# Kernel optimization log

Measured on AMD Instinct MI355X. Metric: run time of the kernel, lower is better.

## Reference

```python
import jax, jax.numpy as jnp
import numpy as np

B, CIN, COUT, L, K, HEADS, GROUPS, EPS = 16, 256, 512, 1024, 3, 8, 32, 1e-5


def group_norm(x, w, b, groups, eps=EPS):
    Bx, C, Lx = x.shape
    g = x.reshape(Bx, groups, C // groups, Lx)
    mu = g.mean(axis=(2, 3), keepdims=True)
    var = g.var(axis=(2, 3), keepdims=True)
    g = (g - mu) * jax.lax.rsqrt(var + eps)
    return g.reshape(Bx, C, Lx) * w[None, :, None] + b[None, :, None]


def conv1d(x, w, b, pad):
    y = jax.lax.conv_general_dilated(x, w, window_strides=(1,), padding=[(pad, pad)],
                                     dimension_numbers=('NCH', 'OIH', 'NCH'))
    return y + b[None, :, None]


def setup_inputs() -> dict:
    key = jax.random.key(0)
    ks = jax.random.split(key, 12)
    def kn(k, shape, fan_in, scale=1.0):
        return (np.sqrt(1.0 / fan_in) * jax.random.normal(k, shape, dtype=jnp.float32)) * scale
    return {
        'x': jax.random.normal(ks[0], (B, CIN, L), dtype=jnp.float32),
        'norm0_w': jnp.ones((CIN,), jnp.float32), 'norm0_b': jnp.zeros((CIN,), jnp.float32),
        'conv0_w': kn(ks[1], (COUT, CIN, K), CIN * K), 'conv0_b': jnp.zeros((COUT,), jnp.float32),
        'norm1_w': jnp.ones((COUT,), jnp.float32), 'norm1_b': jnp.zeros((COUT,), jnp.float32),
        'conv1_w': kn(ks[2], (COUT, COUT, K), COUT * K, 1e-5), 'conv1_b': jnp.zeros((COUT,), jnp.float32),
        'skip_w': kn(ks[3], (COUT, CIN, 1), CIN), 'skip_b': jnp.zeros((COUT,), jnp.float32),
        'norm2_w': jnp.ones((COUT,), jnp.float32), 'norm2_b': jnp.zeros((COUT,), jnp.float32),
        'qkv_w': kn(ks[4], (COUT * 3, COUT, 1), COUT), 'qkv_b': jnp.zeros((COUT * 3,), jnp.float32),
        'proj_w': kn(ks[5], (COUT, COUT, 1), COUT, 1e-5), 'proj_b': jnp.zeros((COUT,), jnp.float32),
    }


def reference(x, norm0_w, norm0_b, conv0_w, conv0_b, norm1_w, norm1_b, conv1_w, conv1_b,
              skip_w, skip_b, norm2_w, norm2_b, qkv_w, qkv_b, proj_w, proj_b):
    orig = x
    h = conv1d(jax.nn.silu(group_norm(x, norm0_w, norm0_b, min(GROUPS, CIN))), conv0_w, conv0_b, (K - 1) // 2)
    h = jax.nn.silu(group_norm(h, norm1_w, norm1_b, min(GROUPS, COUT)))
    h = conv1d(h, conv1_w, conv1_b, (K - 1) // 2)
    h = h + conv1d(orig, skip_w, skip_b, 0)  # skip (in != out), dropout p=0
    # skip_scale = 1
    # attention: qkv [B, 3C, L] -> [B*H, C/H, 3, L] (channel axis splits as H, C/H, 3)
    qkv = conv1d(group_norm(h, norm2_w, norm2_b, min(GROUPS, COUT)), qkv_w, qkv_b, 0)
    ch = COUT // HEADS
    qkv = qkv.reshape(B * HEADS, ch, 3, L)
    q, k, v = qkv[:, :, 0], qkv[:, :, 1], qkv[:, :, 2]  # each [BH, ch, L]
    scores = jnp.einsum('nci,ncj->nij', q, k) / np.sqrt(ch).astype(np.float32)
    attn = jax.nn.softmax(scores, axis=-1)
    a = jnp.einsum('nij,ncj->nci', attn, v).reshape(B, COUT, L)
    return h + conv1d(a, proj_w, proj_b, 0)
```

## Files before the change

kernel.cpp:

```cpp
#include <hip/hip_runtime.h>


typedef float f32x4 __attribute__((ext_vector_type(4)));
typedef float f32x16 __attribute__((ext_vector_type(16)));
typedef short short8 __attribute__((ext_vector_type(8)));

__device__ __forceinline__ unsigned short f2bf(float f) {
  union { float f; unsigned u; } v; v.f = f;
  return (unsigned short)((v.u + 0x7FFFu + ((v.u >> 16) & 1u)) >> 16);
}
__device__ __forceinline__ float bf2f(unsigned short h) {
  union { unsigned u; float f; } v; v.u = ((unsigned)h) << 16;
  return v.f;
}

__device__ __forceinline__ float fexp2(float x) {
  float r;
  asm("v_exp_f32 %0, %1" : "=v"(r) : "v"(x));
  return r;
}

__device__ __forceinline__ void gload_lds16(const void* g, void* l) {
  __builtin_amdgcn_global_load_lds(
      (const __attribute__((address_space(1))) unsigned int*)g,
      (__attribute__((address_space(3))) unsigned int*)l, 16, 0, 0);
}

__device__ __forceinline__ float swap_add(float x) {
  float a = x, b = x;
  asm("v_permlane32_swap_b32 %0, %1" : "+v"(a), "+v"(b));
  return a + b;
}

__device__ __forceinline__ short8 pack8(float a0, float a1, float a2, float a3,
                                        float a4, float a5, float a6, float a7) {
  unsigned x0, x1, x2, x3;
  asm("v_cvt_pk_bf16_f32 %0, %1, %2" : "=v"(x0) : "v"(a0), "v"(a1));
  asm("v_cvt_pk_bf16_f32 %0, %1, %2" : "=v"(x1) : "v"(a2), "v"(a3));
  asm("v_cvt_pk_bf16_f32 %0, %1, %2" : "=v"(x2) : "v"(a4), "v"(a5));
  asm("v_cvt_pk_bf16_f32 %0, %1, %2" : "=v"(x3) : "v"(a6), "v"(a7));
  asm("v_permlane32_swap_b32 %0, %1" : "+v"(x0), "+v"(x2));
  asm("v_permlane32_swap_b32 %0, %1" : "+v"(x1), "+v"(x3));
  union { unsigned u[4]; short8 s; } r;
  r.u[0] = x0; r.u[1] = x1; r.u[2] = x2; r.u[3] = x3;
  return r.s;
}
#define PACK8(V, B) pack8(V[B+0], V[B+1], V[B+2], V[B+3], V[B+4], V[B+5], V[B+6], V[B+7])

__global__ __launch_bounds__(256) void prep_stats(
    const float* __restrict__ c0w, const float* __restrict__ c1w,
    const float* __restrict__ skw, const float* __restrict__ qw,
    const float* __restrict__ pw,
    unsigned short* __restrict__ WT0, unsigned short* __restrict__ WT1,
    unsigned short* __restrict__ WSK, unsigned short* __restrict__ WQ,
    unsigned short* __restrict__ WP,
    const float* __restrict__ x, float2* __restrict__ mr,
    unsigned short* __restrict__ outT) {
  __shared__ float2 red[4];
  const int t = threadIdx.x;
  if (blockIdx.x >= 9216) {
    const int blk = blockIdx.x - 9216;
    const int g = blk & 31;
    const int bb = blk >> 5;
    const size_t base = ((size_t)bb * 256 + g * 8) * 1024;
    float s = 0.f, ss = 0.f;
#pragma unroll
    for (int i = t * 4; i < 8192; i += 1024) {
      const float4 v = *(const float4*)(x + base + i);
      s += (v.x + v.y) + (v.z + v.w);
      ss += (v.x * v.x + v.y * v.y) + (v.z * v.z + v.w * v.w);
    }
#pragma unroll
    for (int off = 32; off; off >>= 1) {
      s += __shfl_down(s, off);
      ss += __shfl_down(ss, off);
    }
    if ((t & 63) == 0) red[t >> 6] = make_float2(s, ss);
    __syncthreads();
    const float2 r0 = red[0], r1 = red[1], r2 = red[2], r3 = red[3];
    const float tots = (r0.x + r1.x) + (r2.x + r3.x);
    const float totss = (r0.y + r1.y) + (r2.y + r3.y);
    const float mean = tots * (1.f / 8192.f);
    const float var = totss * (1.f / 8192.f) - mean * mean;
    if (t == 0) mr[bb * 32 + g] = make_float2(mean, rsqrtf(var + 1e-5f));
    unsigned short* ob = outT + (size_t)bb * 1026 * 256 + g * 8;
    if (t < 8) {
      ob[t] = 0;
      ob[(size_t)1025 * 256 + t] = 0;
    }
    return;
  }
  int idx = blockIdx.x * 256 + t;
  if (idx < 393216) {
    const int ci = idx & 255; const int rem = idx >> 8;
    const int co = rem & 511; const int kk = rem >> 9;
    WT0[idx] = f2bf(c0w[((size_t)co * 256 + ci) * 3 + kk]); return;
  }
  idx -= 393216;
  if (idx < 786432) {
    const int ci = idx & 511; const int rem = idx >> 9;
    const int co = rem & 511; const int kk = rem >> 9;
    WT1[idx] = f2bf(c1w[((size_t)co * 512 + ci) * 3 + kk]); return;
  }
  idx -= 786432;
  if (idx < 131072) { WSK[idx] = f2bf(skw[idx]); return; }
  idx -= 131072;
  if (idx < 786432) {
    const int ci = idx & 511; const int m = idx >> 9;
    const int s = m >> 9, rem = m & 511, h = rem >> 6, c = rem & 63;
    WQ[idx] = f2bf(qw[((size_t)(h * 192 + c * 3 + s) * 512) + ci]); return;
  }
  idx -= 786432;
  WP[idx] = f2bf(pw[idx]);
}

template<int MODE, bool SILU, int C, bool PADZ, bool RAW, bool IN16>
__global__ __launch_bounds__(256) void nt_kernel(
    const float* __restrict__ in, const float2* __restrict__ st,
    const float* __restrict__ gw, const float* __restrict__ gb,
    unsigned short* __restrict__ outT, unsigned short* __restrict__ rawT) {
  constexpr int CPG = C / 32;
  __shared__ float ls[64][65];
  __shared__ unsigned short lsr[RAW ? 64 : 1][72];
  __shared__ float2 gstat[4];
  const int b = blockIdx.z, c0 = blockIdx.y * 64, l0 = blockIdx.x * 64;
  const int t = threadIdx.x;
  if (MODE == 2) {
    if (t < 4) {
      const int g = (c0 >> 4) + t;
      const float2* p = st + (((size_t)b * 4 + (g >> 3)) * 8 + (g & 7)) * 8;
      float s = 0.f, ss = 0.f;
#pragma unroll
      for (int i = 0; i < 8; ++i) { s += p[i].x; ss += p[i].y; }
      const float mean = s * (1.f / 16384.f);
      const float var = ss * (1.f / 16384.f) - mean * mean;
      gstat[t] = make_float2(mean, rsqrtf(var + 1e-5f));
    }
    __syncthreads();
  }
  const int lw = (t & 15) * 4;
  const int cr = t >> 4;
#pragma unroll
  for (int p = 0; p < 4; ++p) {
    const int c = p * 16 + cr;
    const int cc = c0 + c;
    float sc = 1.f, bi = 0.f;
    if (MODE == 1) {
      const float2 ms = st[b * 32 + cc / CPG];
      sc = gw[cc] * ms.y;
      bi = gb[cc] - ms.x * sc;
    } else if (MODE == 2) {
      const float2 ms = gstat[c >> 4];
      sc = gw[cc] * ms.y;
      bi = gb[cc] - ms.x * sc;
    }
    float4 v;
    if (IN16) {
      const ushort4 u4 = *(const ushort4*)((const unsigned short*)in +
                                           ((size_t)b * C + cc) * 1024 + l0 + lw);
      v = make_float4(bf2f(u4.x), bf2f(u4.y), bf2f(u4.z), bf2f(u4.w));
    } else {
      v = *(const float4*)(in + ((size_t)b * C + cc) * 1024 + l0 + lw);
    }
    if (RAW) {
      lsr[c][lw + 0] = f2bf(v.x);
      lsr[c][lw + 1] = f2bf(v.y);
      lsr[c][lw + 2] = f2bf(v.z);
      lsr[c][lw + 3] = f2bf(v.w);
    }
    float o[4] = {v.x * sc + bi, v.y * sc + bi, v.z * sc + bi, v.w * sc + bi};
    if (SILU) {
#pragma unroll
      for (int d = 0; d < 4; ++d) o[d] = o[d] / (1.f + __expf(-o[d]));
    }
#pragma unroll
    for (int d = 0; d < 4; ++d) ls[c][lw + d] = o[d];
  }
  __syncthreads();
  const int l = t >> 2, c16 = (t & 3) * 16;
  short8 v0, v1;
#pragma unroll
  for (int j = 0; j < 8; ++j) v0[j] = (short)f2bf(ls[c16 + j][l]);
#pragma unroll
  for (int j = 0; j < 8; ++j) v1[j] = (short)f2bf(ls[c16 + 8 + j][l]);
  unsigned short* ob = outT + ((size_t)b * 1026 + l0 + l + 1) * C + c0 + c16;
  *(short8*)ob = v0;
  *(short8*)(ob + 8) = v1;
  if (RAW) {
    short8 w0, w1;
#pragma unroll
    for (int j = 0; j < 8; ++j) w0[j] = (short)lsr[c16 + j][l];
#pragma unroll
    for (int j = 0; j < 8; ++j) w1[j] = (short)lsr[c16 + 8 + j][l];
    unsigned short* rb = rawT + ((size_t)b * 1026 + l0 + l + 1) * C + c0 + c16;
    *(short8*)rb = w0;
    *(short8*)(rb + 8) = w1;
  }
  if (PADZ) {
    const short8 z = {};
    if (blockIdx.x == 0 && t < 8)
      *(short8*)(outT + (size_t)b * 1026 * C + c0 + t * 8) = z;
    if (blockIdx.x == 15 && t < 8)
      *(short8*)(outT + ((size_t)b * 1026 + 1025) * C + c0 + t * 8) = z;
  }
}

__global__ __launch_bounds__(256) void ntE_kernel(
    const unsigned short* __restrict__ Ht, const float2* __restrict__ part,
    const float* __restrict__ gw, const float* __restrict__ gb,
    unsigned short* __restrict__ outT) {
  __shared__ float2 gstat[32];
  const int b = blockIdx.y;
  const int t = threadIdx.x;
  if (t < 32) {
    const float2* p = part + (((size_t)b * 4 + (t >> 3)) * 8 + (t & 7)) * 8;
    float s = 0.f, ss = 0.f;
#pragma unroll
    for (int i = 0; i < 8; ++i) { s += p[i].x; ss += p[i].y; }
    const float mean = s * (1.f / 16384.f);
    const float var = ss * (1.f / 16384.f) - mean * mean;
    gstat[t] = make_float2(mean, rsqrtf(var + 1e-5f));
  }
  __syncthreads();
  const int c8 = t & 63;
  const float2 ms = gstat[c8 >> 1];
  const int cbase = c8 * 8;
  const float4 g0 = *(const float4*)(gw + cbase);
  const float4 g1 = *(const float4*)(gw + cbase + 4);
  const float4 b0 = *(const float4*)(gb + cbase);
  const float4 b1 = *(const float4*)(gb + cbase + 4);
  float sc[8], bi[8];
  sc[0] = g0.x * ms.y; sc[1] = g0.y * ms.y; sc[2] = g0.z * ms.y; sc[3] = g0.w * ms.y;
  sc[4] = g1.x * ms.y; sc[5] = g1.y * ms.y; sc[6] = g1.z * ms.y; sc[7] = g1.w * ms.y;
  bi[0] = b0.x - ms.x * sc[0]; bi[1] = b0.y - ms.x * sc[1];
  bi[2] = b0.z - ms.x * sc[2]; bi[3] = b0.w - ms.x * sc[3];
  bi[4] = b1.x - ms.x * sc[4]; bi[5] = b1.y - ms.x * sc[5];
  bi[6] = b1.z - ms.x * sc[6]; bi[7] = b1.w - ms.x * sc[7];
#pragma unroll
  for (int pass = 0; pass < 4; ++pass) {
    const int lp = blockIdx.x * 16 + pass * 4 + (t >> 6) + 1;
    const size_t o = ((size_t)b * 1026 + lp) * 512 + cbase;
    const short8 v = *(const short8*)(Ht + o);
    short8 r;
#pragma unroll
    for (int e = 0; e < 8; ++e) {
      const float y = bf2f((unsigned short)v[e]) * sc[e] + bi[e];
      r[e] = (short)f2bf(y / (1.f + __expf(-y)));
    }
    *(short8*)(outT + o) = r;
  }
  const short8 z = {};
  if (blockIdx.x == 0 && t < 64)
    *(short8*)(outT + (size_t)b * 1026 * 512 + t * 8) = z;
  if (blockIdx.x == 63 && t < 64)
    *(short8*)(outT + ((size_t)b * 1026 + 1025) * 512 + t * 8) = z;
}

template<int K, bool ADD, bool SCATTER, bool FUSE, bool STATS, bool TROUT,
         bool OUT16, bool ADD16>
__global__ __launch_bounds__(256, 2) void convmm_kernel(
    const unsigned short* __restrict__ Xt, const unsigned short* __restrict__ Wt,
    const float* __restrict__ bias, const float* __restrict__ addsrc,
    float* __restrict__ outp,
    unsigned short* __restrict__ qd, unsigned short* __restrict__ kd,
    unsigned short* __restrict__ vd, int Cin, int Cout,
    const unsigned short* __restrict__ X2, const unsigned short* __restrict__ W2,
    const float* __restrict__ bias2, int Cin2, float2* __restrict__ part) {
  constexpr int XR = (K == 3) ? 160 : 128;
  __shared__ __align__(16) unsigned short smem[K * 128 * 64 + XR * 64];
  unsigned short* wT = smem;
  unsigned short* xT = smem + K * 128 * 64;
  const int t = threadIdx.x, lane = t & 63, w = t >> 6;
  const int b = blockIdx.z, co0 = blockIdx.y * 128, l0 = blockIdx.x * 128;
  const int m0 = (w >> 1) * 64, n0 = (w & 1) * 64;
  const int START = (K == 3) ? l0 : (l0 + 1);
  f32x4 acc[4][4] = {};
  for (int ci0 = 0; ci0 < Cin; ci0 += 64) {
    __syncthreads();
    for (int rr = 0; rr < K * 4; ++rr) {
      const int row = rr * 32 + (t >> 3);
      const int co = row & 127;
      const int c16 = (t & 7) ^ (co & 7);
      gload_lds16(Wt + ((size_t)(row >> 7) * Cout + co0 + co) * Cin + ci0 + c16 * 8,
                  (char*)wT + (rr * 256 + t) * 16);
    }
    for (int rr = 0; rr < XR / 32; ++rr) {
      const int r = rr * 32 + (t >> 3);
      int lp = START + r;
      if (lp > 1025) lp = 1025;
      const int c16 = (t & 7) ^ (r & 7);
      gload_lds16(Xt + ((size_t)b * 1026 + lp) * Cin + ci0 + c16 * 8,
                  (char*)xT + (rr * 256 + t) * 16);
    }
    __syncthreads();
#pragma unroll
    for (int kk = 0; kk < K; ++kk) {
#pragma unroll
      for (int ks = 0; ks < 2; ++ks) {
        short8 af[4], bfr[4];
#pragma unroll
        for (int mf = 0; mf < 4; ++mf) {
          const int row = m0 + mf * 16 + (lane & 15);
          const int u = (kk * 128 + row) * 8 + ((ks * 4 + (lane >> 4)) ^ (row & 7));
          af[mf] = *(const short8*)(wT + u * 8);
        }
#pragma unroll
        for (int nf = 0; nf < 4; ++nf) {
          const int r = n0 + nf * 16 + (lane & 15) + kk;
          const int u = r * 8 + ((ks * 4 + (lane >> 4)) ^ (r & 7));
          bfr[nf] = *(const short8*)(xT + u * 8);
        }
#pragma unroll
        for (int mf = 0; mf < 4; ++mf)
#pragma unroll
          for (int nf = 0; nf < 4; ++nf)
            acc[mf][nf] = __builtin_amdgcn_mfma_f32_16x16x32_bf16(
                af[mf], bfr[nf], acc[mf][nf], 0, 0, 0);
      }
    }
  }
  if (FUSE) {
    for (int ci0 = 0; ci0 < Cin2; ci0 += 64) {
      __syncthreads();
      for (int rr = 0; rr < 4; ++rr) {
        const int co = rr * 32 + (t >> 3);
        const int c16 = (t & 7) ^ (co & 7);
        gload_lds16(W2 + (size_t)(co0 + co) * Cin2 + ci0 + c16 * 8,
                    (char*)wT + (rr * 256 + t) * 16);
      }
      for (int rr = 0; rr < 4; ++rr) {
        const int r = rr * 32 + (t >> 3);
        const int lp = l0 + 1 + r;
        const int c16 = (t & 7) ^ (r & 7);
        gload_lds16(X2 + ((size_t)b * 1026 + lp) * Cin2 + ci0 + c16 * 8,
                    (char*)xT + (rr * 256 + t) * 16);
      }
      __syncthreads();
#pragma unroll
      for (int ks = 0; ks < 2; ++ks) {
        short8 af[4], bfr[4];
#pragma unroll
        for (int mf = 0; mf < 4; ++mf) {
          const int row = m0 + mf * 16 + (lane & 15);
          const int u = row * 8 + ((ks * 4 + (lane >> 4)) ^ (row & 7));
          af[mf] = *(const short8*)(wT + u * 8);
        }
#pragma unroll
        for (int nf = 0; nf < 4; ++nf) {
          const int r = n0 + nf * 16 + (lane & 15);
          const int u = r * 8 + ((ks * 4 + (lane >> 4)) ^ (r & 7));
          bfr[nf] = *(const short8*)(xT + u * 8);
        }
#pragma unroll
        for (int mf = 0; mf < 4; ++mf)
#pragma unroll
          for (int nf = 0; nf < 4; ++nf)
            acc[mf][nf] = __builtin_amdgcn_mfma_f32_16x16x32_bf16(
                af[mf], bfr[nf], acc[mf][nf], 0, 0, 0);
      }
    }
  }
  if (TROUT) {
    __syncthreads();
    unsigned short* TP = smem;
    float2* sr = (float2*)(TP + 128 * 128);
    float sg[4] = {}, ssg[4] = {};
#pragma unroll
    for (int mf = 0; mf < 4; ++mf)
#pragma unroll
      for (int r = 0; r < 4; ++r) {
        const int mloc = m0 + mf * 16 + (lane >> 4) * 4 + r;
        const float bv = bias[co0 + mloc];
#pragma unroll
        for (int nf = 0; nf < 4; ++nf) {
          const int l = n0 + nf * 16 + (lane & 15);
          const float v = acc[mf][nf][r] + bv;
          sg[mf] += v; ssg[mf] += v * v;
          const int u = l * 16 + ((mloc >> 3) ^ (l & 7));
          TP[u * 8 + (mloc & 7)] = f2bf(v);
        }
      }
#pragma unroll
    for (int mf = 0; mf < 4; ++mf) {
      float s = sg[mf], ss = ssg[mf];
#pragma unroll
      for (int off = 32; off; off >>= 1) {
        s += __shfl_down(s, off);
        ss += __shfl_down(ss, off);
      }
      if (lane == 0)
        sr[(((w >> 1) * 4 + mf) << 1) | (w & 1)] = make_float2(s, ss);
    }
    __syncthreads();
    for (int it = 0; it < 8; ++it) {
      const int idx = it * 256 + t;
      const int l = idx >> 4, mu = idx & 15;
      const short8 v = *(const short8*)(TP + (l * 16 + (mu ^ (l & 7))) * 8);
      *(short8*)(qd + ((size_t)b * 1026 + l0 + l + 1) * 512 + co0 + mu * 8) = v;
    }
    if (t < 8) {
      const float2 a = sr[t * 2], c = sr[t * 2 + 1];
      part[(((size_t)b * 4 + blockIdx.y) * 8 + t) * 8 + blockIdx.x] =
          make_float2(a.x + c.x, a.y + c.y);
    }
  } else if (!SCATTER) {
    float sg[4] = {}, ssg[4] = {};
#pragma unroll
    for (int mf = 0; mf < 4; ++mf) {
#pragma unroll
      for (int r = 0; r < 4; ++r) {
        const int co = co0 + m0 + mf * 16 + (lane >> 4) * 4 + r;
        float bv = bias[co];
        if (FUSE) bv += bias2[co];
#pragma unroll
        for (int nf = 0; nf < 4; ++nf) {
          const int l = l0 + n0 + nf * 16 + (lane & 15);
          const size_t o = ((size_t)b * Cout + co) * 1024 + l;
          float v = acc[mf][nf][r] + bv;
          if (ADD) {
            if (ADD16) v += bf2f(((const unsigned short*)addsrc)[o]);
            else       v += addsrc[o];
          }
          if (OUT16) ((unsigned short*)outp)[o] = f2bf(v);
          else       outp[o] = v;
          if (STATS) { sg[mf] += v; ssg[mf] += v * v; }
        }
      }
    }
    if (STATS) {
      __syncthreads();
      float2* sr = (float2*)smem;
#pragma unroll
      for (int mf = 0; mf < 4; ++mf) {
        float s = sg[mf], ss = ssg[mf];
#pragma unroll
        for (int off = 32; off; off >>= 1) {
          s += __shfl_down(s, off);
          ss += __shfl_down(ss, off);
        }
        if (lane == 0)
          sr[(((w >> 1) * 4 + mf) << 1) | (w & 1)] = make_float2(s, ss);
      }
      __syncthreads();
      if (t < 8) {
        const float2 a = sr[t * 2], c = sr[t * 2 + 1];
        part[(((size_t)b * 4 + blockIdx.y) * 8 + t) * 8 + blockIdx.x] =
            make_float2(a.x + c.x, a.y + c.y);
      }
    }
  } else {
    __syncthreads();
    unsigned short* TP = smem;
    const int sidx = co0 >> 9;
    const int mbase = co0 & 511;
    const float qscale = (sidx == 0) ? 0.18033688f : 1.0f;
    if (sidx < 2) {
#pragma unroll
      for (int mf = 0; mf < 4; ++mf)
#pragma unroll
        for (int r = 0; r < 4; ++r) {
          const int mloc = m0 + mf * 16 + (lane >> 4) * 4 + r;
          const int mg = mbase + mloc;
          const float bv = bias[(mg >> 6) * 192 + (mg & 63) * 3 + sidx];
#pragma unroll
          for (int nf = 0; nf < 4; ++nf) {
            const int l = n0 + nf * 16 + (lane & 15);
            const int u = l * 16 + ((mloc >> 3) ^ (l & 7));
            TP[u * 8 + (mloc & 7)] = f2bf((acc[mf][nf][r] + bv) * qscale);
          }
        }
      __syncthreads();
      unsigned short* dst = (sidx == 0) ? qd : kd;
      for (int it = 0; it < 8; ++it) {
        const int idx = it * 256 + t;
        const int l = idx >> 4, mu = idx & 15;
        const int mg = mbase + mu * 8;
        const int bh = b * 8 + (mg >> 6);
        const short8 v = *(const short8*)(TP + (l * 16 + (mu ^ (l & 7))) * 8);
        *(short8*)(dst + ((size_t)bh * 1024 + l0 + l) * 64 + (mg & 63)) = v;
      }
    } else {
#pragma unroll
      for (int mf = 0; mf < 4; ++mf)
#pragma unroll
        for (int r = 0; r < 4; ++r) {
          const int mloc = m0 + mf * 16 + (lane >> 4) * 4 + r;
          const int mg = mbase + mloc;
          const float bv = bias[(mg >> 6) * 192 + (mg & 63) * 3 + 2];
#pragma unroll
          for (int nf = 0; nf < 4; ++nf) {
            const int l = n0 + nf * 16 + (lane & 15);
            const int u = mloc * 16 + ((l >> 3) ^ ((mloc & 7) << 1));
            TP[u * 8 + (l & 7)] = f2bf(acc[mf][nf][r] + bv);
          }
        }
      __syncthreads();
      for (int it = 0; it < 8; ++it) {
        const int idx = it * 256 + t;
        const int mloc = idx >> 4, lu = idx & 15;
        const int mg = mbase + mloc;
        const int bh = b * 8 + (mg >> 6);
        const short8 v =
            *(const short8*)(TP + (mloc * 16 + (lu ^ ((mloc & 7) << 1))) * 8);
        *(short8*)(vd + ((size_t)bh * 64 + (mg & 63)) * 1024 + l0 + lu * 8) = v;
      }
    }
  }
}

__global__ __launch_bounds__(256, 2) void attn_mfma(
    const unsigned short* __restrict__ Qb, const unsigned short* __restrict__ Kb,
    const unsigned short* __restrict__ Vb, unsigned short* __restrict__ Ab) {
  __shared__ __align__(16) unsigned short Ks[2][64 * 64];
  __shared__ __align__(16) unsigned short Vs[2][64 * 64];
  unsigned short* QP = &Ks[0][0];
  const int t = threadIdx.x, lane = t & 63, w = t >> 6;
  const int hi = lane >> 5, l31 = lane & 31;
  const int id = blockIdx.x;
  const int xcd = id & 7, local = id >> 3;
  const int bh = (xcd << 4) | (local >> 2);
  const int b = bh >> 3, h = bh & 7;
  const int iq0 = (local & 3) * 256;
  const unsigned short* Qg = Qb + ((size_t)bh * 1024 + iq0) * 64;
  const unsigned short* Kg = Kb + (size_t)bh * 1024 * 64;
  const unsigned short* Vg = Vb + (size_t)bh * 64 * 1024;
  for (int rr = 0; rr < 8; ++rr) {
    const int r = rr * 32 + (t >> 3), c16 = (t & 7) ^ (r & 7);
    gload_lds16(Qg + (size_t)r * 64 + c16 * 8, (char*)QP + (rr * 256 + t) * 16);
  }
  __syncthreads();
  const int irow0 = w * 64 + l31;
  const int irow1 = w * 64 + 32 + l31;
  short8 qf[2][4];
#pragma unroll
  for (int kc = 0; kc < 4; ++kc) {
    const int u0 = irow0 * 8 + ((kc * 2 + hi) ^ (irow0 & 7));
    const int u1 = irow1 * 8 + ((kc * 2 + hi) ^ (irow1 & 7));
    qf[0][kc] = *(const short8*)(QP + u0 * 8);
    qf[1][kc] = *(const short8*)(QP + u1 * 8);
  }
  __syncthreads();
  for (int rr = 0; rr < 2; ++rr) {
    const int r = rr * 32 + (t >> 3), c16 = (t & 7) ^ (r & 7);
    gload_lds16(Kg + (size_t)r * 64 + c16 * 8, (char*)Ks[0] + (rr * 256 + t) * 16);
    gload_lds16(Vg + (size_t)r * 1024 + c16 * 8, (char*)Vs[0] + (rr * 256 + t) * 16);
  }
  __syncthreads();
  float ls0 = 0.f, ls1 = 0.f;
  f32x16 oA[2][2] = {};
  auto kv_iter = [&](const int ti, const int cur) {
    if (ti < 15) {
      const int j1 = (ti + 1) * 64;
      for (int rr = 0; rr < 2; ++rr) {
        const int r = rr * 32 + (t >> 3), c16 = (t & 7) ^ (r & 7);
        gload_lds16(Kg + (size_t)(j1 + r) * 64 + c16 * 8,
                    (char*)Ks[cur ^ 1] + (rr * 256 + t) * 16);
        gload_lds16(Vg + (size_t)r * 1024 + j1 + c16 * 8,
                    (char*)Vs[cur ^ 1] + (rr * 256 + t) * 16);
      }
    }
    f32x16 s00 = {}, s01 = {}, s10 = {}, s11 = {};
    __builtin_amdgcn_s_setprio(1);
#pragma unroll
    for (int kc = 0; kc < 4; ++kc) {
      const int r0 = l31, r1 = 32 + l31;
      const short8 k0 = *(const short8*)(Ks[cur] + (r0 * 8 + ((kc * 2 + hi) ^ (r0 & 7))) * 8);
      const short8 k1 = *(const short8*)(Ks[cur] + (r1 * 8 + ((kc * 2 + hi) ^ (r1 & 7))) * 8);
      s00 = __builtin_amdgcn_mfma_f32_32x32x16_bf16(k0, qf[0][kc], s00, 0, 0, 0);
      s01 = __builtin_amdgcn_mfma_f32_32x32x16_bf16(k1, qf[0][kc], s01, 0, 0, 0);
      s10 = __builtin_amdgcn_mfma_f32_32x32x16_bf16(k0, qf[1][kc], s10, 0, 0, 0);
      s11 = __builtin_amdgcn_mfma_f32_32x32x16_bf16(k1, qf[1][kc], s11, 0, 0, 0);
    }
    __builtin_amdgcn_s_setprio(0);
    short8 pb0[4], pb1[4];
    {
      float p0 = 0.f, p1 = 0.f, p2 = 0.f, p3 = 0.f;
#pragma unroll
      for (int r = 0; r < 16; ++r) { s00[r] = fexp2(s00[r]); }
#pragma unroll
      for (int r = 0; r < 16; r += 4) {
        p0 += s00[r + 0]; p1 += s00[r + 1]; p2 += s00[r + 2]; p3 += s00[r + 3];
      }
#pragma unroll
      for (int r = 0; r < 16; ++r) { s01[r] = fexp2(s01[r]); }
#pragma unroll
      for (int r = 0; r < 16; r += 4) {
        p0 += s01[r + 0]; p1 += s01[r + 1]; p2 += s01[r + 2]; p3 += s01[r + 3];
      }
      ls0 += (p0 + p1) + (p2 + p3);
      pb0[0] = PACK8(s00, 0); pb0[1] = PACK8(s00, 8);
      pb0[2] = PACK8(s01, 0); pb0[3] = PACK8(s01, 8);
    }
    {
      float p0 = 0.f, p1 = 0.f, p2 = 0.f, p3 = 0.f;
#pragma unroll
      for (int r = 0; r < 16; ++r) { s10[r] = fexp2(s10[r]); }
#pragma unroll
      for (int r = 0; r < 16; r += 4) {
        p0 += s10[r + 0]; p1 += s10[r + 1]; p2 += s10[r + 2]; p3 += s10[r + 3];
      }
#pragma unroll
      for (int r = 0; r < 16; ++r) { s11[r] = fexp2(s11[r]); }
#pragma unroll
      for (int r = 0; r < 16; r += 4) {
        p0 += s11[r + 0]; p1 += s11[r + 1]; p2 += s11[r + 2]; p3 += s11[r + 3];
      }
      ls1 += (p0 + p1) + (p2 + p3);
      pb1[0] = PACK8(s10, 0); pb1[1] = PACK8(s10, 8);
      pb1[2] = PACK8(s11, 0); pb1[3] = PACK8(s11, 8);
    }
    __builtin_amdgcn_s_setprio(1);
#pragma unroll
    for (int cf = 0; cf < 2; ++cf) {
      const int row = cf * 32 + l31;
#pragma unroll
      for (int s = 0; s < 4; ++s) {
        const int u = row * 8 + ((s * 2 + hi) ^ (row & 7));
        const short8 va = *(const short8*)(Vs[cur] + u * 8);
        oA[0][cf] = __builtin_amdgcn_mfma_f32_32x32x16_bf16(va, pb0[s], oA[0][cf], 0, 0, 0);
        oA[1][cf] = __builtin_amdgcn_mfma_f32_32x32x16_bf16(va, pb1[s], oA[1][cf], 0, 0, 0);
      }
    }
    __builtin_amdgcn_s_setprio(0);
    __syncthreads();
  };
  for (int ti = 0; ti < 16; ti += 2) {
    kv_iter(ti, 0);
    kv_iter(ti + 1, 1);
  }
  const float inv0 = 1.f / swap_add(ls0);
  const float inv1 = 1.f / swap_add(ls1);
#pragma unroll
  for (int f = 0; f < 2; ++f) {
    const int irow = f ? irow1 : irow0;
    const float inv = f ? inv1 : inv0;
#pragma unroll
    for (int cf = 0; cf < 2; ++cf)
#pragma unroll
      for (int r = 0; r < 16; ++r) {
        const int c = cf * 32 + (r & 3) + 8 * (r >> 2) + 4 * hi;
        const int u = irow * 8 + ((c >> 3) ^ (irow & 7));
        QP[u * 8 + (c & 7)] = f2bf(oA[f][cf][r] * inv);
      }
  }
  for (int rr = 0; rr < 8; ++rr) {
    const int row = w * 64 + rr * 8 + (lane >> 3);
    const int c16 = lane & 7;
    const int u = row * 8 + (c16 ^ (row & 7));
    const short8 vv = *(const short8*)(QP + u * 8);
    *(short8*)(Ab + ((size_t)b * 1026 + iq0 + row + 1) * 512 + h * 64 + c16 * 8) = vv;
  }
}

#define MB(x) ((size_t)(x) << 20)

extern "C" void kernel_launch(void* const* d_in, const int* in_sizes, int n_in,
                              void* d_out, int out_size, void* d_ws,
                              size_t ws_size, hipStream_t stream) {
  const float* x   = (const float*)d_in[0];
  const float* n0w = (const float*)d_in[1];
  const float* n0b = (const float*)d_in[2];
  const float* c0w = (const float*)d_in[3];
  const float* c0b = (const float*)d_in[4];
  const float* n1w = (const float*)d_in[5];
  const float* n1b = (const float*)d_in[6];
  const float* c1w = (const float*)d_in[7];
  const float* c1b = (const float*)d_in[8];
  const float* skw = (const float*)d_in[9];
  const float* skb = (const float*)d_in[10];
  const float* n2w = (const float*)d_in[11];
  const float* n2b = (const float*)d_in[12];
  const float* qw  = (const float*)d_in[13];
  const float* qb  = (const float*)d_in[14];
  const float* pw  = (const float*)d_in[15];
  const float* pb  = (const float*)d_in[16];
  char* wsb = (char*)d_ws;
  unsigned short* WT0 = (unsigned short*)(wsb);
  unsigned short* WT1 = (unsigned short*)(wsb + MB(1));
  unsigned short* WSK = (unsigned short*)(wsb + MB(3));
  unsigned short* WQ  = (unsigned short*)(wsb + MB(4));
  unsigned short* WP  = (unsigned short*)(wsb + MB(6));
  unsigned short* H2b = (unsigned short*)(wsb + MB(7));
  unsigned short* Qb2 = (unsigned short*)(wsb + MB(41));
  unsigned short* Kb2 = (unsigned short*)(wsb + MB(58));
  unsigned short* H0t = (unsigned short*)(wsb + MB(75));
  unsigned short* Vb2 = (unsigned short*)(wsb + MB(75));
  unsigned short* Xt2 = (unsigned short*)(wsb + MB(92));
  unsigned short* Xt0 = (unsigned short*)(wsb + MB(109));
  unsigned short* Xt1 = (unsigned short*)(wsb + MB(109));
  unsigned short* Ab  = (unsigned short*)(wsb + MB(109));
  unsigned short* Xbf = (unsigned short*)(wsb + MB(126));
  float2* MR0   = (float2*)(wsb + MB(135));
  float2* PART1 = (float2*)(wsb + MB(135) + 8192);
  float2* PART2 = (float2*)(wsb + MB(135) + 32768);
  float* outp = (float*)d_out;

  prep_stats<<<9728, 256, 0, stream>>>(c0w, c1w, skw, qw, pw,
                                       WT0, WT1, WSK, WQ, WP, x, MR0, Xt0);
  nt_kernel<1, true, 256, false, true, false><<<dim3(16, 4, 16), 256, 0, stream>>>(
      x, MR0, n0w, n0b, Xt0, Xbf);
  convmm_kernel<3, false, false, false, true, true, false, false>
      <<<dim3(8, 4, 16), 256, 0, stream>>>(
      Xt0, WT0, c0b, nullptr, nullptr, H0t, nullptr, nullptr, 256, 512,
      nullptr, nullptr, nullptr, 0, PART1);
  ntE_kernel<<<dim3(64, 16), 256, 0, stream>>>(H0t, PART1, n1w, n1b, Xt1);
  convmm_kernel<3, false, false, true, true, false, true, false>
      <<<dim3(8, 4, 16), 256, 0, stream>>>(
      Xt1, WT1, c1b, nullptr, (float*)H2b, nullptr, nullptr, nullptr, 512, 512,
      Xbf, WSK, skb, 256, PART2);
  nt_kernel<2, false, 512, false, false, true><<<dim3(16, 8, 16), 256, 0, stream>>>(
      (const float*)H2b, PART2, n2w, n2b, Xt2, nullptr);
  convmm_kernel<1, false, true, false, false, false, false, false>
      <<<dim3(8, 12, 16), 256, 0, stream>>>(
      Xt2, WQ, qb, nullptr, nullptr, Qb2, Kb2, Vb2, 512, 1536,
      nullptr, nullptr, nullptr, 0, nullptr);
  attn_mfma<<<dim3(512), 256, 0, stream>>>(Qb2, Kb2, Vb2, Ab);
  convmm_kernel<1, true, false, false, false, false, false, true>
      <<<dim3(8, 4, 16), 256, 0, stream>>>(
      Ab, WP, pb, (const float*)H2b, outp, nullptr, nullptr, nullptr, 512, 512,
      nullptr, nullptr, nullptr, 0, nullptr);
}
```

Before: 176.3 us.

## Double-buffer K=1 conv GEMM loads and interleave softmax with PV MFMAs

For the K=1 (pointwise) conv GEMM path, shared-memory staging becomes double-buffered. The next 64-channel slice is prefetched while MFMAs run on the current one, and one barrier per step replaces the two used before. In the attention inner loop, V fragments are loaded once up front and the first PV MFMA batch is issued before the second softmax exp block, so exp work can overlap matrix ops. The setprio hints around PV are dropped. The costs are more LDS per block (which may limit occupancy) and higher register pressure from holding all V fragments.

Result: slower. 184.7 us (+4.8%).

```diff
diff --git a/kernel.cpp b/kernel.cpp
--- a/kernel.cpp
+++ b/kernel.cpp
@@ -266,76 +266,40 @@
     unsigned short* __restrict__ vd, int Cin, int Cout,
     const unsigned short* __restrict__ X2, const unsigned short* __restrict__ W2,
     const float* __restrict__ bias2, int Cin2, float2* __restrict__ part) {
-  constexpr int XR = (K == 3) ? 160 : 128;
-  __shared__ __align__(16) unsigned short smem[K * 128 * 64 + XR * 64];
-  unsigned short* wT = smem;
-  unsigned short* xT = smem + K * 128 * 64;
+  constexpr int XR = 160;
+  constexpr int SMEM_SHORTS = (K == 3) ? (3 * 128 * 64 + XR * 64)
+                                       : (2 * (128 * 64 + 128 * 64));
+  __shared__ __align__(16) unsigned short smem[SMEM_SHORTS];
   const int t = threadIdx.x, lane = t & 63, w = t >> 6;
   const int b = blockIdx.z, co0 = blockIdx.y * 128, l0 = blockIdx.x * 128;
   const int m0 = (w >> 1) * 64, n0 = (w & 1) * 64;
-  const int START = (K == 3) ? l0 : (l0 + 1);
   f32x4 acc[4][4] = {};
-  for (int ci0 = 0; ci0 < Cin; ci0 += 64) {
-    __syncthreads();
-    for (int rr = 0; rr < K * 4; ++rr) {
-      const int row = rr * 32 + (t >> 3);
-      const int co = row & 127;
-      const int c16 = (t & 7) ^ (co & 7);
-      gload_lds16(Wt + ((size_t)(row >> 7) * Cout + co0 + co) * Cin + ci0 + c16 * 8,
-                  (char*)wT + (rr * 256 + t) * 16);
-    }
-    for (int rr = 0; rr < XR / 32; ++rr) {
-      const int r = rr * 32 + (t >> 3);
-      int lp = START + r;
-      if (lp > 1025) lp = 1025;
-      const int c16 = (t & 7) ^ (r & 7);
-      gload_lds16(Xt + ((size_t)b * 1026 + lp) * Cin + ci0 + c16 * 8,
-                  (char*)xT + (rr * 256 + t) * 16);
-    }
-    __syncthreads();
-#pragma unroll
-    for (int kk = 0; kk < K; ++kk) {
-#pragma unroll
-      for (int ks = 0; ks < 2; ++ks) {
-        short8 af[4], bfr[4];
-#pragma unroll
-        for (int mf = 0; mf < 4; ++mf) {
-          const int row = m0 + mf * 16 + (lane & 15);
-          const int u = (kk * 128 + row) * 8 + ((ks * 4 + (lane >> 4)) ^ (row & 7));
-          af[mf] = *(const short8*)(wT + u * 8);
-        }
-#pragma unroll
-        for (int nf = 0; nf < 4; ++nf) {
-          const int r = n0 + nf * 16 + (lane & 15) + kk;
-          const int u = r * 8 + ((ks * 4 + (lane >> 4)) ^ (r & 7));
-          bfr[nf] = *(const short8*)(xT + u * 8);
-        }
-#pragma unroll
-        for (int mf = 0; mf < 4; ++mf)
-#pragma unroll
-          for (int nf = 0; nf < 4; ++nf)
-            acc[mf][nf] = __builtin_amdgcn_mfma_f32_16x16x32_bf16(
-                af[mf], bfr[nf], acc[mf][nf], 0, 0, 0);
-      }
-    }
-  }
-  if (FUSE) {
-    for (int ci0 = 0; ci0 < Cin2; ci0 += 64) {
-      __syncthreads();
+  if constexpr (K == 1) {
+    auto stage = [&](int buf, int ci0) {
+      unsigned short* wB = smem + buf * 16384;
+      unsigned short* xB = wB + 8192;
       for (int rr = 0; rr < 4; ++rr) {
-        const int co = rr * 32 + (t >> 3);
-        const int c16 = (t & 7) ^ (co & 7);
-        gload_lds16(W2 + (size_t)(co0 + co) * Cin2 + ci0 + c16 * 8,
-                    (char*)wT + (rr * 256 + t) * 16);
+        const int row = rr * 32 + (t >> 3);
+        const int c16 = (t & 7) ^ (row & 7);
+        gload_lds16(Wt + (size_t)(co0 + row) * Cin + ci0 + c16 * 8,
+                    (char*)wB + (rr * 256 + t) * 16);
       }
       for (int rr = 0; rr < 4; ++rr) {
         const int r = rr * 32 + (t >> 3);
         const int lp = l0 + 1 + r;
         const int c16 = (t & 7) ^ (r & 7);
-        gload_lds16(X2 + ((size_t)b * 1026 + lp) * Cin2 + ci0 + c16 * 8,
-                    (char*)xT + (rr * 256 + t) * 16);
-      }
-      __syncthreads();
+        gload_lds16(Xt + ((size_t)b * 1026 + lp) * Cin + ci0 + c16 * 8,
+                    (char*)xB + (rr * 256 + t) * 16);
+      }
+    };
+    stage(0, 0);
+    __syncthreads();
+    const int nsteps = Cin >> 6;
+    for (int step = 0; step < nsteps; ++step) {
+      const int cur = step & 1;
+      if (step + 1 < nsteps) stage(cur ^ 1, (step + 1) << 6);
+      const unsigned short* wT = smem + cur * 16384;
+      const unsigned short* xT = wT + 8192;
 #pragma unroll
       for (int ks = 0; ks < 2; ++ks) {
         short8 af[4], bfr[4];
@@ -357,6 +321,96 @@
           for (int nf = 0; nf < 4; ++nf)
             acc[mf][nf] = __builtin_amdgcn_mfma_f32_16x16x32_bf16(
                 af[mf], bfr[nf], acc[mf][nf], 0, 0, 0);
+      }
+      __syncthreads();
+    }
+  } else {
+    unsigned short* wT = smem;
+    unsigned short* xT = smem + K * 128 * 64;
+    const int START = l0;
+    for (int ci0 = 0; ci0 < Cin; ci0 += 64) {
+      __syncthreads();
+      for (int rr = 0; rr < K * 4; ++rr) {
+        const int row = rr * 32 + (t >> 3);
+        const int co = row & 127;
+        const int c16 = (t & 7) ^ (co & 7);
+        gload_lds16(Wt + ((size_t)(row >> 7) * Cout + co0 + co) * Cin + ci0 + c16 * 8,
+                    (char*)wT + (rr * 256 + t) * 16);
+      }
+      for (int rr = 0; rr < XR / 32; ++rr) {
+        const int r = rr * 32 + (t >> 3);
+        int lp = START + r;
+        if (lp > 1025) lp = 1025;
+        const int c16 = (t & 7) ^ (r & 7);
+        gload_lds16(Xt + ((size_t)b * 1026 + lp) * Cin + ci0 + c16 * 8,
+                    (char*)xT + (rr * 256 + t) * 16);
+      }
+      __syncthreads();
+#pragma unroll
+      for (int kk = 0; kk < K; ++kk) {
+#pragma unroll
+        for (int ks = 0; ks < 2; ++ks) {
+          short8 af[4], bfr[4];
+#pragma unroll
+          for (int mf = 0; mf < 4; ++mf) {
+            const int row = m0 + mf * 16 + (lane & 15);
+            const int u = (kk * 128 + row) * 8 + ((ks * 4 + (lane >> 4)) ^ (row & 7));
+            af[mf] = *(const short8*)(wT + u * 8);
+          }
+#pragma unroll
+          for (int nf = 0; nf < 4; ++nf) {
+            const int r = n0 + nf * 16 + (lane & 15) + kk;
+            const int u = r * 8 + ((ks * 4 + (lane >> 4)) ^ (r & 7));
+            bfr[nf] = *(const short8*)(xT + u * 8);
+          }
+#pragma unroll
+          for (int mf = 0; mf < 4; ++mf)
+#pragma unroll
+            for (int nf = 0; nf < 4; ++nf)
+              acc[mf][nf] = __builtin_amdgcn_mfma_f32_16x16x32_bf16(
+                  af[mf], bfr[nf], acc[mf][nf], 0, 0, 0);
+        }
+      }
+    }
+    if (FUSE) {
+      for (int ci0 = 0; ci0 < Cin2; ci0 += 64) {
+        __syncthreads();
+        for (int rr = 0; rr < 4; ++rr) {
+          const int co = rr * 32 + (t >> 3);
+          const int c16 = (t & 7) ^ (co & 7);
+          gload_lds16(W2 + (size_t)(co0 + co) * Cin2 + ci0 + c16 * 8,
+                      (char*)wT + (rr * 256 + t) * 16);
+        }
+        for (int rr = 0; rr < 4; ++rr) {
+          const int r = rr * 32 + (t >> 3);
+          const int lp = l0 + 1 + r;
+          const int c16 = (t & 7) ^ (r & 7);
+          gload_lds16(X2 + ((size_t)b * 1026 + lp) * Cin2 + ci0 + c16 * 8,
+                      (char*)xT + (rr * 256 + t) * 16);
+        }
+        __syncthreads();
+#pragma unroll
+        for (int ks = 0; ks < 2; ++ks) {
+          short8 af[4], bfr[4];
+#pragma unroll
+          for (int mf = 0; mf < 4; ++mf) {
+            const int row = m0 + mf * 16 + (lane & 15);
+            const int u = row * 8 + ((ks * 4 + (lane >> 4)) ^ (row & 7));
+            af[mf] = *(const short8*)(wT + u * 8);
+          }
+#pragma unroll
+          for (int nf = 0; nf < 4; ++nf) {
+            const int r = n0 + nf * 16 + (lane & 15);
+            const int u = r * 8 + ((ks * 4 + (lane >> 4)) ^ (r & 7));
+            bfr[nf] = *(const short8*)(xT + u * 8);
+          }
+#pragma unroll
+          for (int mf = 0; mf < 4; ++mf)
+#pragma unroll
+            for (int nf = 0; nf < 4; ++nf)
+              acc[mf][nf] = __builtin_amdgcn_mfma_f32_16x16x32_bf16(
+                  af[mf], bfr[nf], acc[mf][nf], 0, 0, 0);
+        }
       }
     }
   }
@@ -572,7 +626,17 @@
       s11 = __builtin_amdgcn_mfma_f32_32x32x16_bf16(k1, qf[1][kc], s11, 0, 0, 0);
     }
     __builtin_amdgcn_s_setprio(0);
-    short8 pb0[4], pb1[4];
+    short8 va[2][4];
+#pragma unroll
+    for (int cf = 0; cf < 2; ++cf) {
+      const int row = cf * 32 + l31;
+#pragma unroll
+      for (int s = 0; s < 4; ++s) {
+        const int u = row * 8 + ((s * 2 + hi) ^ (row & 7));
+        va[cf][s] = *(const short8*)(Vs[cur] + u * 8);
+      }
+    }
+    short8 pb0[4];
     {
       float p0 = 0.f, p1 = 0.f, p2 = 0.f, p3 = 0.f;
 #pragma unroll
@@ -591,6 +655,12 @@
       pb0[0] = PACK8(s00, 0); pb0[1] = PACK8(s00, 8);
       pb0[2] = PACK8(s01, 0); pb0[3] = PACK8(s01, 8);
     }
+#pragma unroll
+    for (int cf = 0; cf < 2; ++cf)
+#pragma unroll
+      for (int s = 0; s < 4; ++s)
+        oA[0][cf] = __builtin_amdgcn_mfma_f32_32x32x16_bf16(va[cf][s], pb0[s], oA[0][cf], 0, 0, 0);
+    short8 pb1[4];
     {
       float p0 = 0.f, p1 = 0.f, p2 = 0.f, p3 = 0.f;
 #pragma unroll
@@ -609,19 +679,11 @@
       pb1[0] = PACK8(s10, 0); pb1[1] = PACK8(s10, 8);
       pb1[2] = PACK8(s11, 0); pb1[3] = PACK8(s11, 8);
     }
-    __builtin_amdgcn_s_setprio(1);
-#pragma unroll
-    for (int cf = 0; cf < 2; ++cf) {
-      const int row = cf * 32 + l31;
-#pragma unroll
-      for (int s = 0; s < 4; ++s) {
-        const int u = row * 8 + ((s * 2 + hi) ^ (row & 7));
-        const short8 va = *(const short8*)(Vs[cur] + u * 8);
-        oA[0][cf] = __builtin_amdgcn_mfma_f32_32x32x16_bf16(va, pb0[s], oA[0][cf], 0, 0, 0);
-        oA[1][cf] = __builtin_amdgcn_mfma_f32_32x32x16_bf16(va, pb1[s], oA[1][cf], 0, 0, 0);
-      }
-    }
-    __builtin_amdgcn_s_setprio(0);
+#pragma unroll
+    for (int cf = 0; cf < 2; ++cf)
+#pragma unroll
+      for (int s = 0; s < 4; ++s)
+        oA[1][cf] = __builtin_amdgcn_mfma_f32_32x32x16_bf16(va[cf][s], pb1[s], oA[1][cf], 0, 0, 0);
     __syncthreads();
   };
   for (int ti = 0; ti < 16; ti += 2) {
```
